# Performance work log

Measured on AMD Instinct MI355X. Metric: run time of the kernel, lower is better.

Reference implementation:

```python
import jax, jax.numpy as jnp
import numpy as np

N_NODES = 50000
N_EDGES = 800000
D_IN = 128
D_OUT = 128
N_MLP = 2


def _lin(x, W, b):
    return x @ W.T + b


def setup_inputs() -> dict:
    key = jax.random.key(0)
    ks = jax.random.split(key, 32)
    d = {}
    d['feat'] = jax.random.normal(ks[0], (N_NODES, D_IN), dtype=jnp.float32)
    d['src'] = jax.random.randint(ks[1], (N_EDGES,), 0, N_NODES, dtype=jnp.int32)
    d['dst'] = jax.random.randint(ks[2], (N_EDGES,), 0, N_NODES, dtype=jnp.int32)
    s_in = 1.0 / np.sqrt(D_IN)
    s_out = 1.0 / np.sqrt(D_OUT)
    i = 3
    def w(shape, s):
        nonlocal i
        out = jax.random.normal(ks[i], shape, dtype=jnp.float32) * s
        i += 1
        return out
    for nm in ['asrc', 'adst', 'asub', 'amul']:
        d['W_' + nm] = w((D_OUT, D_IN), s_in)
        d['b_' + nm] = w((D_OUT,), s_in)
    d['W_aout'] = w((1, D_OUT), s_out)
    d['b_aout'] = w((1,), s_out)
    for nm in ['pool', 'pool2']:
        d['W_' + nm] = w((D_IN, D_IN), s_in)
        d['b_' + nm] = w((D_IN,), s_in)
    for nm in ['self', 'neigh', 'neigh2']:
        d['W_' + nm] = w((D_OUT, D_IN), s_in)
        d['b_' + nm] = w((D_OUT,), s_in)
    d['W_mlp'] = w((N_MLP, D_OUT, D_OUT), s_out)
    d['b_mlp'] = w((N_MLP, D_OUT), s_out)
    return d


def reference(feat, src, dst,
              W_asrc, b_asrc, W_adst, b_adst, W_asub, b_asub, W_amul, b_amul,
              W_aout, b_aout, W_pool, b_pool, W_pool2, b_pool2,
              W_self, b_self, W_neigh, b_neigh, W_neigh2, b_neigh2,
              W_mlp, b_mlp):
    gelu = lambda x: jax.nn.gelu(x, approximate=False)
    fs = feat[src]            # [E, D_IN] gathered source feats
    fd = feat[dst]            # [E, D_IN] gathered dest feats
    # edge attention score
    e = _lin(fs - fd, W_asub, b_asub) + _lin(fs * fd, W_amul, b_amul)
    e = e + _lin(feat, W_asrc, b_asrc)[src] + _lin(feat, W_adst, b_adst)[dst]
    e = gelu(e)
    e = jax.nn.leaky_relu(_lin(e, W_aout, b_aout), 0.2)  # [E, 1]
    deg = jax.ops.segment_sum(jnp.ones((src.shape[0],), jnp.float32), dst,
                              num_segments=N_NODES)      # in-degree
    has_in = (deg > 0)[:, None]
    # max-pool branch
    h = gelu(_lin(feat, W_pool, b_pool))
    m = e * h[src]
    neigh = jax.ops.segment_max(m, dst, num_segments=N_NODES)
    neigh = jnp.where(has_in, neigh, 0.0)
    # mean-pool branch
    h2 = gelu(_lin(feat, W_pool2, b_pool2))
    m2 = e * h2[src]
    neigh2 = jax.ops.segment_sum(m2, dst, num_segments=N_NODES)
    neigh2 = neigh2 / jnp.maximum(deg, 1.0)[:, None]
    rst = _lin(feat, W_self, b_self) + _lin(neigh, W_neigh, b_neigh) \
        + _lin(neigh2, W_neigh2, b_neigh2)
    for li in range(W_mlp.shape[0]):
        rst = rst + _lin(gelu(rst), W_mlp[li], b_mlp[li])
    return rst
```

## Files before the change

### kernel.cpp

```cpp
#include <hip/hip_runtime.h>
#include <cstdint>
#include <cstddef>

#define NN 50000
#define NE 800000
#define DD 128

#define NBK 391
#define BSLOT 4096

static_assert(NN % 16 == 0, "node tiles");
static_assert(NE % 16 == 0, "edge tiles");
static_assert(((NN + 127) >> 7) == NBK, "bucket count");

typedef _Float16 h16_t;
typedef h16_t h16x8 __attribute__((ext_vector_type(8)));
typedef h16_t h16x4 __attribute__((ext_vector_type(4)));
typedef float f32x4 __attribute__((ext_vector_type(4)));
typedef float f32x16 __attribute__((ext_vector_type(16)));

__device__ __forceinline__ float gelu_f(float x) {
    float u = x * x;
    float t = fmaf(u, -0.1029442445f, -2.3021184019f);
    float s = __builtin_amdgcn_exp2f(x * t);
    return x * __builtin_amdgcn_rcpf(1.0f + s);
}

__device__ __forceinline__ int frag_idx(int ch, int k) {
    int t = ch >> 4, n = ch & 15;
    int kb = k >> 5, r = k & 31, q = r >> 3, j = r & 7;
    return ((((t * 4 + kb) * 4 + q) * 16 + n) << 3) + j;
}

__device__ __forceinline__ int frag32_idx(int ch, int k) {
    int t = ch >> 5, m = ch & 31;
    int kc = k >> 4, q = (k >> 3) & 1, j = k & 7;
    return ((((t * 8 + kc) * 2 + q) * 32 + m) << 3) + j;
}

__global__ __launch_bounds__(256) void convert_feat_kernel(
    const float* __restrict__ feat, h16_t* __restrict__ fb)
{
    int i = blockIdx.x * 256 + threadIdx.x;
    f32x4 v = ((const f32x4*)feat)[i];
    h16x4 o;
    o[0] = (h16_t)v[0]; o[1] = (h16_t)v[1]; o[2] = (h16_t)v[2]; o[3] = (h16_t)v[3];
    ((h16x4*)fb)[i] = o;
}

__global__ __launch_bounds__(256) void prep_kernel(
    const float* __restrict__ W_asrc, const float* __restrict__ b_asrc,
    const float* __restrict__ W_adst, const float* __restrict__ b_adst,
    const float* __restrict__ W_asub, const float* __restrict__ b_asub,
    const float* __restrict__ W_amul, const float* __restrict__ b_amul,
    const float* __restrict__ W_pool, const float* __restrict__ W_pool2,
    const float* __restrict__ W_self, const float* __restrict__ b_self,
    const float* __restrict__ W_neigh, const float* __restrict__ b_neigh,
    const float* __restrict__ W_neigh2, const float* __restrict__ b_neigh2,
    const float* __restrict__ W_mlp,
    h16_t* __restrict__ W_Sf, h16_t* __restrict__ W_Df, h16_t* __restrict__ W_amulf,
    h16_t* __restrict__ W_poolf, h16_t* __restrict__ W_pool2f,
    h16_t* __restrict__ W_selff, h16_t* __restrict__ W_neighf, h16_t* __restrict__ W_neigh2f,
    h16_t* __restrict__ W_mlpf,
    float* __restrict__ b_e, float* __restrict__ b_rst)
{
    int gid = blockIdx.x * 256 + threadIdx.x;
    float sub = W_asub[gid];
    int ch = gid >> 7, k = gid & 127;
    int fi = frag_idx(ch, k);
    W_Sf[fi] = (h16_t)(W_asrc[gid] + sub);
    W_Df[fi] = (h16_t)(W_adst[gid] - sub);
    W_amulf[frag32_idx(ch, k)] = (h16_t)W_amul[gid];
    W_poolf[fi]   = (h16_t)W_pool[gid];
    W_pool2f[fi]  = (h16_t)W_pool2[gid];
    W_selff[fi]   = (h16_t)W_self[gid];
    W_neighf[fi]  = (h16_t)W_neigh[gid];
    W_neigh2f[fi] = (h16_t)W_neigh2[gid];
    W_mlpf[fi]            = (h16_t)W_mlp[gid];
    W_mlpf[DD * DD + fi]  = (h16_t)W_mlp[DD * DD + gid];
    if (gid < DD) {
        b_e[gid]   = b_asub[gid] + b_amul[gid] + b_asrc[gid] + b_adst[gid];
        b_rst[gid] = b_self[gid] + b_neigh[gid] + b_neigh2[gid];
    }
}

__global__ __launch_bounds__(256) void scatter_bucket_kernel(
    const int* __restrict__ src, const int* __restrict__ dst,
    int* __restrict__ gcursor, int2* __restrict__ ebuf)
{
    __shared__ int cnt[NBK];
    __shared__ int ofs[NBK];
    int t = threadIdx.x;
    for (int b = t; b < NBK; b += 256) cnt[b] = 0;
    __syncthreads();
    int qbase = blockIdx.x * 1024 + t;
    int4 s4[4], d4[4];
    bool valid[4];
#pragma unroll
    for (int k = 0; k < 4; k++) {
        int q = qbase + k * 256;
        valid[k] = q < NE / 4;
        if (valid[k]) {
            s4[k] = ((const int4*)src)[q];
            d4[k] = ((const int4*)dst)[q];
#pragma unroll
            for (int j = 0; j < 4; j++)
                atomicAdd(&cnt[((&d4[k].x)[j]) >> 7], 1);
        }
    }
    __syncthreads();
    for (int b = t; b < NBK; b += 256) {
        int c = cnt[b];
        ofs[b] = c ? atomicAdd(&gcursor[b], c) : 0;
    }
    __syncthreads();
#pragma unroll
    for (int k = 0; k < 4; k++) {
        if (valid[k]) {
#pragma unroll
            for (int j = 0; j < 4; j++) {
                int d = (&d4[k].x)[j];
                int b = d >> 7;
                int p = atomicAdd(&ofs[b], 1);
                int2 pk;
                pk.x = (&s4[k].x)[j];
                pk.y = d;
                ebuf[(size_t)b * BSLOT + p] = pk;
            }
        }
    }
}

__global__ __launch_bounds__(256) void finalize_csr_kernel(
    const int2* __restrict__ ebuf, const int* __restrict__ gcursor,
    int2* __restrict__ csr, int* __restrict__ offsets, int* __restrict__ deg)
{
    __shared__ int lcnt[128];
    __shared__ int nbase[128];
    __shared__ int pre[128];
    __shared__ int redbuf[256];
    int B = blockIdx.x, t = threadIdx.x;
    int v0 = B << 7;
    int cnt = gcursor[B];
    int partial = 0;
    for (int i = t; i < B; i += 256) partial += gcursor[i];
    redbuf[t] = partial;
    __syncthreads();
#pragma unroll
    for (int d = 128; d > 0; d >>= 1) {
        if (t < d) redbuf[t] += redbuf[t + d];
        __syncthreads();
    }
    int dbase = redbuf[0];
    const int2* eb = ebuf + (size_t)B * BSLOT;
    if (t < 128) lcnt[t] = 0;
    __syncthreads();
    for (int i = t; i < cnt; i += 256)
        atomicAdd(&lcnt[eb[i].y - v0], 1);
    __syncthreads();
    int c = (t < 128) ? lcnt[t] : 0;
    if (t < 128) pre[t] = c;
    __syncthreads();
#pragma unroll
    for (int d = 1; d < 128; d <<= 1) {
        int x = (t >= d && t < 128) ? pre[t - d] : 0;
        __syncthreads();
        if (t < 128) pre[t] += x;
        __syncthreads();
    }
    if (t < 128) {
        int nb = dbase + pre[t] - c;
        nbase[t] = nb;
        int v = v0 + t;
        if (v < NN) { offsets[v] = nb; deg[v] = c; }
        lcnt[t] = 0;
    }
    __syncthreads();
    for (int i = t; i < cnt; i += 256) {
        int2 pk = eb[i];
        int j = pk.y - v0;
        int pos = nbase[j] + atomicAdd(&lcnt[j], 1);
        csr[pos] = pk;
    }
}

template <bool GELU>
__device__ __forceinline__ void mm16_to_lds(
    const h16x8 a[4], const h16_t* __restrict__ Wf, const float* __restrict__ bias,
    h16_t* __restrict__ L, int n, int q, int lane)
{
#pragma unroll
    for (int t = 0; t < 8; t++) {
        f32x4 acc = {0.f, 0.f, 0.f, 0.f};
#pragma unroll
        for (int kb = 0; kb < 4; kb++) {
            h16x8 b = *(const h16x8*)(Wf + (((t * 4 + kb) * 64 + lane) << 3));
            acc = __builtin_amdgcn_mfma_f32_16x16x32_f16(a[kb], b, acc, 0, 0, 0);
        }
        int ch = t * 16 + n;
        float bv = bias ? bias[ch] : 0.0f;
#pragma unroll
        for (int r = 0; r < 4; r++) {
            float v = acc[r] + bv;
            L[(q * 4 + r) * 136 + ch] = (h16_t)(GELU ? gelu_f(v) : v);
        }
    }
}

__global__ __launch_bounds__(256) void node_linear_kernel(
    const h16_t* __restrict__ fb,
    const h16_t* __restrict__ W_poolf, const float* __restrict__ b_pool,
    const h16_t* __restrict__ W_pool2f, const float* __restrict__ b_pool2,
    const h16_t* __restrict__ W_Sf, const float* __restrict__ b_e,
    const h16_t* __restrict__ W_Df,
    h16_t* __restrict__ hh, h16_t* __restrict__ us, h16_t* __restrict__ ud)
{
    __shared__ __align__(16) h16_t Lh[4][16 * 136];
    __shared__ __align__(16) h16_t Lh2[4][16 * 136];
    int wave = threadIdx.x >> 6;
    int wid = blockIdx.x * 4 + wave;
    if (wid >= NN / 16) return;
    int lane = threadIdx.x & 63, n = lane & 15, q = lane >> 4;
    int nb = wid * 16;
    h16_t* lh = Lh[wave];
    h16_t* lh2 = Lh2[wave];
    h16x8 a[4];
#pragma unroll
    for (int kb = 0; kb < 4; kb++)
        a[kb] = *(const h16x8*)(fb + (size_t)(nb + n) * DD + kb * 32 + q * 8);

    mm16_to_lds<true>(a, W_poolf, b_pool, lh, n, q, lane);
    mm16_to_lds<true>(a, W_pool2f, b_pool2, lh2, n, q, lane);
    __builtin_amdgcn_wave_barrier();
#pragma unroll
    for (int i = 0; i < 8; i++) {
        int r = 2 * i + (lane >> 5);
        int c = lane & 31;
        h16x4 xh = *(const h16x4*)(lh + r * 136 + 4 * c);
        h16x4 x2 = *(const h16x4*)(lh2 + r * 136 + 4 * c);
        h16x8 o;
        o[0] = xh[0]; o[1] = xh[1]; o[2] = x2[0]; o[3] = x2[1];
        o[4] = xh[2]; o[5] = xh[3]; o[6] = x2[2]; o[7] = x2[3];
        *(h16x8*)(hh + (size_t)(nb + r) * 256 + 8 * c) = o;
    }
    __builtin_amdgcn_wave_barrier();
    mm16_to_lds<false>(a, W_Sf, b_e, lh, n, q, lane);
    __builtin_amdgcn_wave_barrier();
#pragma unroll
    for (int i = 0; i < 4; i++) {
        int r = 4 * i + (lane >> 4);
        int c = lane & 15;
        *(h16x8*)(us + (size_t)(nb + r) * 128 + 8 * c) = *(const h16x8*)(lh + r * 136 + 8 * c);
    }
    __builtin_amdgcn_wave_barrier();
    mm16_to_lds<false>(a, W_Df, nullptr, lh, n, q, lane);
    __builtin_amdgcn_wave_barrier();
#pragma unroll
    for (int i = 0; i < 4; i++) {
        int r = 4 * i + (lane >> 4);
        int c = lane & 15;
        *(h16x8*)(ud + (size_t)(nb + r) * 128 + 8 * c) = *(const h16x8*)(lh + r * 136 + 8 * c);
    }
}

#define ES_NBLK 2500
#define ES_ITERS (NE / 32 / ES_NBLK)

__global__ __launch_bounds__(256, 4) void edge_score_kernel(
    const h16_t* __restrict__ fb,
    const h16_t* __restrict__ us, const h16_t* __restrict__ ud,
    const h16_t* __restrict__ W_amulf,
    const float* __restrict__ w_aout, const float* __restrict__ b_aout,
    int2* __restrict__ csr)
{
    __shared__ __align__(16) h16_t sP[32 * 128];
    __shared__ __align__(16) h16_t sU[32 * 128];
    __shared__ float partials[32 * 5];
    __shared__ float sWa[128];
    int tid = threadIdx.x;
    int wave = tid >> 6, lane = tid & 63;
    int n = lane & 31, q = lane >> 5;
    int t = wave;

    if (tid < 128) sWa[tid] = w_aout[tid];

    h16x8 wAm[8];
#pragma unroll
    for (int kc = 0; kc < 8; kc++)
        wAm[kc] = *(const h16x8*)(W_amulf + ((((t * 8 + kc) * 2 + q) * 32 + n) << 3));
    float bout = b_aout[0];

    int sed0 = tid >> 4, sc = tid & 15;

    int e0 = blockIdx.x * 32;
    int2 pk0 = csr[e0 + sed0];
    int2 pk1 = csr[e0 + sed0 + 16];
    h16x8 pfs0 = *(const h16x8*)(fb + (size_t)pk0.x * DD + sc * 8);
    h16x8 pfd0 = *(const h16x8*)(fb + (size_t)pk0.y * DD + sc * 8);
    h16x8 pus0 = *(const h16x8*)(us + (size_t)pk0.x * DD + sc * 8);
    h16x8 pud0 = *(const h16x8*)(ud + (size_t)pk0.y * DD + sc * 8);
    h16x8 pfs1 = *(const h16x8*)(fb + (size_t)pk1.x * DD + sc * 8);
    h16x8 pfd1 = *(const h16x8*)(fb + (size_t)pk1.y * DD + sc * 8);
    h16x8 pus1 = *(const h16x8*)(us + (size_t)pk1.x * DD + sc * 8);
    h16x8 pud1 = *(const h16x8*)(ud + (size_t)pk1.y * DD + sc * 8);

    for (int it = 0; it < ES_ITERS; it++) {
        int eb = (blockIdx.x + it * ES_NBLK) * 32;
        {
            h16x8 pp = pfs0 * pfd0;
            h16x8 uu = pus0 + pud0;
            int ph = (sc ^ (sed0 & 7)) << 3;
            *(h16x8*)(sP + sed0 * 128 + ph) = pp;
            *(h16x8*)(sU + sed0 * 128 + ph) = uu;
        }
        {
            int ed = sed0 + 16;
            h16x8 pp = pfs1 * pfd1;
            h16x8 uu = pus1 + pud1;
            int ph = (sc ^ (ed & 7)) << 3;
            *(h16x8*)(sP + ed * 128 + ph) = pp;
            *(h16x8*)(sU + ed * 128 + ph) = uu;
        }
        __syncthreads();
        if (it + 1 < ES_ITERS) {
            int e1 = (blockIdx.x + (it + 1) * ES_NBLK) * 32;
            pk0 = csr[e1 + sed0];
            pk1 = csr[e1 + sed0 + 16];
            pfs0 = *(const h16x8*)(fb + (size_t)pk0.x * DD + sc * 8);
            pfd0 = *(const h16x8*)(fb + (size_t)pk0.y * DD + sc * 8);
            pus0 = *(const h16x8*)(us + (size_t)pk0.x * DD + sc * 8);
            pud0 = *(const h16x8*)(ud + (size_t)pk0.y * DD + sc * 8);
            pfs1 = *(const h16x8*)(fb + (size_t)pk1.x * DD + sc * 8);
            pfd1 = *(const h16x8*)(fb + (size_t)pk1.y * DD + sc * 8);
            pus1 = *(const h16x8*)(us + (size_t)pk1.x * DD + sc * 8);
            pud1 = *(const h16x8*)(ud + (size_t)pk1.y * DD + sc * 8);
        }
        f32x16 acc = {};
        int swz = n & 7;
#pragma unroll
        for (int kc = 0; kc < 8; kc++) {
            h16x8 bP = *(const h16x8*)(sP + n * 128 + (((kc * 2 + q) ^ swz) << 3));
            acc = __builtin_amdgcn_mfma_f32_32x32x16_f16(wAm[kc], bP, acc, 0, 0, 0);
        }
        float psum = 0.f;
#pragma unroll
        for (int c = 0; c < 4; c++) {
            h16x4 sv = *(const h16x4*)(sU + n * 128 + (((t * 4 + c) ^ swz) << 3) + q * 4);
            f32x4 wv = *(const f32x4*)(sWa + t * 32 + c * 8 + q * 4);
#pragma unroll
            for (int j = 0; j < 4; j++)
                psum = fmaf(gelu_f(acc[c * 4 + j] + (float)sv[j]), wv[j], psum);
        }
        psum += __shfl_xor(psum, 32, 64);
        if (lane < 32) partials[lane * 5 + wave] = psum;
        __syncthreads();
        if (wave == (it & 3) && lane < 32) {
            const float* pr = partials + lane * 5;
            float s = pr[0] + pr[1] + pr[2] + pr[3] + bout;
            s = s > 0.f ? s : 0.2f * s;
            csr[eb + lane].y = __float_as_int(s);
        }
    }
}

__global__ __launch_bounds__(256) void aggregate_kernel(
    const h16_t* __restrict__ hh,
    const int* __restrict__ offsets, const int* __restrict__ deg,
    const int2* __restrict__ csr,
    h16_t* __restrict__ neigh, h16_t* __restrict__ neigh2)
{
    int wave = threadIdx.x >> 6, lane = threadIdx.x & 63;
    int v = blockIdx.x * 4 + wave;
    if (v >= NN) return;
    int off = offsets[v];
    int dg = deg[v];
    int quarter = lane >> 4;
    int cl = lane & 15;
    float mx[8], sm[8];
#pragma unroll
    for (int j = 0; j < 8; j++) { mx[j] = -INFINITY; sm[j] = 0.f; }
    for (int base = 0; base < dg; base += 64) {
        int cnt = dg - base; if (cnt > 64) cnt = 64;
        int s_l = 0; float sc_l = 0.f;
        if (lane < cnt) {
            int2 pk = csr[off + base + lane];
            s_l = pk.x;
            sc_l = __int_as_float(pk.y);
        }
        int nit = (cnt + 3) >> 2;
#pragma unroll 2
        for (int i = 0; i < nit; i++) {
            int idx = 4 * i + quarter;
            int s = __shfl(s_l, idx, 64);
            float sc = __shfl(sc_l, idx, 64);
            if (idx < cnt) {
                const h16_t* row = hh + (size_t)s * 256 + 16 * cl;
                h16x8 h0 = *(const h16x8*)(row);
                h16x8 h1 = *(const h16x8*)(row + 8);
                mx[0] = fmaxf(mx[0], sc * (float)h0[0]);
                mx[1] = fmaxf(mx[1], sc * (float)h0[1]);
                sm[0] = fmaf(sc, (float)h0[2], sm[0]);
                sm[1] = fmaf(sc, (float)h0[3], sm[1]);
                mx[2] = fmaxf(mx[2], sc * (float)h0[4]);
                mx[3] = fmaxf(mx[3], sc * (float)h0[5]);
                sm[2] = fmaf(sc, (float)h0[6], sm[2]);
                sm[3] = fmaf(sc, (float)h0[7], sm[3]);
                mx[4] = fmaxf(mx[4], sc * (float)h1[0]);
                mx[5] = fmaxf(mx[5], sc * (float)h1[1]);
                sm[4] = fmaf(sc, (float)h1[2], sm[4]);
                sm[5] = fmaf(sc, (float)h1[3], sm[5]);
                mx[6] = fmaxf(mx[6], sc * (float)h1[4]);
                mx[7] = fmaxf(mx[7], sc * (float)h1[5]);
                sm[6] = fmaf(sc, (float)h1[6], sm[6]);
                sm[7] = fmaf(sc, (float)h1[7], sm[7]);
            }
        }
    }
#pragma unroll
    for (int j = 0; j < 8; j++) {
        mx[j] = fmaxf(mx[j], __shfl_xor(mx[j], 16, 64));
        mx[j] = fmaxf(mx[j], __shfl_xor(mx[j], 32, 64));
        sm[j] += __shfl_xor(sm[j], 16, 64);
        sm[j] += __shfl_xor(sm[j], 32, 64);
    }
    if (quarter == 0) {
        float inv = 1.0f / (float)(dg > 1 ? dg : 1);
        h16x8 n1, n2;
#pragma unroll
        for (int j = 0; j < 8; j++) {
            n1[j] = (h16_t)(dg > 0 ? mx[j] : 0.0f);
            n2[j] = (h16_t)(sm[j] * inv);
        }
        *(h16x8*)(neigh + (size_t)v * DD + 8 * cl) = n1;
        *(h16x8*)(neigh2 + (size_t)v * DD + 8 * cl) = n2;
    }
}

__global__ __launch_bounds__(256) void final_kernel(
    const h16_t* __restrict__ fb, const h16_t* __restrict__ neigh, const h16_t* __restrict__ neigh2,
    const h16_t* __restrict__ W_selff, const h16_t* __restrict__ W_neighf, const h16_t* __restrict__ W_neigh2f,
    const float* __restrict__ b_rst,
    const h16_t* __restrict__ W_mlpf, const float* __restrict__ b_mlp,
    float* __restrict__ out)
{
    __shared__ __align__(16) float lds[4][16 * 132];
    int wave = threadIdx.x >> 6;
    int wid = blockIdx.x * 4 + wave;
    if (wid >= NN / 16) return;
    int lane = threadIdx.x & 63, n = lane & 15, q = lane >> 4;
    int nb = wid * 16;
    float* L = lds[wave];

    h16x8 af[4], an[4], am[4];
#pragma unroll
    for (int kb = 0; kb < 4; kb++) {
        size_t o = (size_t)(nb + n) * DD + kb * 32 + q * 8;
        af[kb] = *(const h16x8*)(fb + o);
        an[kb] = *(const h16x8*)(neigh + o);
        am[kb] = *(const h16x8*)(neigh2 + o);
    }
    f32x4 rst[8];
#pragma unroll
    for (int t = 0; t < 8; t++) {
        f32x4 acc = {0.f, 0.f, 0.f, 0.f};
#pragma unroll
        for (int kb = 0; kb < 4; kb++) {
            int wo = ((t * 4 + kb) * 64 + lane) << 3;
            acc = __builtin_amdgcn_mfma_f32_16x16x32_f16(af[kb], *(const h16x8*)(W_selff + wo), acc, 0, 0, 0);
            acc = __builtin_amdgcn_mfma_f32_16x16x32_f16(an[kb], *(const h16x8*)(W_neighf + wo), acc, 0, 0, 0);
            acc = __builtin_amdgcn_mfma_f32_16x16x32_f16(am[kb], *(const h16x8*)(W_neigh2f + wo), acc, 0, 0, 0);
        }
        float bv = b_rst[t * 16 + n];
#pragma unroll
        for (int r = 0; r < 4; r++) acc[r] += bv;
        rst[t] = acc;
    }

#pragma unroll
    for (int li = 0; li < 2; li++) {
#pragma unroll
        for (int t = 0; t < 8; t++)
#pragma unroll
            for (int r = 0; r < 4; r++)
                L[(q * 4 + r) * 132 + t * 16 + n] = gelu_f(rst[t][r]);
        __builtin_amdgcn_wave_barrier();
        h16x8 g[4];
#pragma unroll
        for (int kb = 0; kb < 4; kb++) {
            const f32x4* p = (const f32x4*)&L[n * 132 + kb * 32 + q * 8];
            f32x4 x0 = p[0], x1 = p[1];
            h16x8 gg;
            gg[0] = (h16_t)x0[0]; gg[1] = (h16_t)x0[1]; gg[2] = (h16_t)x0[2]; gg[3] = (h16_t)x0[3];
            gg[4] = (h16_t)x1[0]; gg[5] = (h16_t)x1[1]; gg[6] = (h16_t)x1[2]; gg[7] = (h16_t)x1[3];
            g[kb] = gg;
        }
        __builtin_amdgcn_wave_barrier();
        const h16_t* Wl = W_mlpf + li * DD * DD;
#pragma unroll
        for (int t = 0; t < 8; t++) {
            f32x4 acc = {0.f, 0.f, 0.f, 0.f};
#pragma unroll
            for (int kb = 0; kb < 4; kb++) {
                h16x8 b = *(const h16x8*)(Wl + (((t * 4 + kb) * 64 + lane) << 3));
                acc = __builtin_amdgcn_mfma_f32_16x16x32_f16(g[kb], b, acc, 0, 0, 0);
            }
            float bm = b_mlp[li * DD + t * 16 + n];
#pragma unroll
            for (int r = 0; r < 4; r++) rst[t][r] += acc[r] + bm;
        }
    }

#pragma unroll
    for (int t = 0; t < 8; t++)
#pragma unroll
        for (int r = 0; r < 4; r++)
            out[(size_t)(nb + q * 4 + r) * DD + t * 16 + n] = rst[t][r];
}

extern "C" void kernel_launch(void* const* d_in, const int* in_sizes, int n_in,
                              void* d_out, int out_size, void* d_ws, size_t ws_size,
                              hipStream_t stream)
{
    const float* feat    = (const float*)d_in[0];
    const int*   src     = (const int*)d_in[1];
    const int*   dst     = (const int*)d_in[2];
    const float* W_asrc  = (const float*)d_in[3],  *b_asrc  = (const float*)d_in[4];
    const float* W_adst  = (const float*)d_in[5],  *b_adst  = (const float*)d_in[6];
    const float* W_asub  = (const float*)d_in[7],  *b_asub  = (const float*)d_in[8];
    const float* W_amul  = (const float*)d_in[9],  *b_amul  = (const float*)d_in[10];
    const float* W_aout  = (const float*)d_in[11], *b_aout  = (const float*)d_in[12];
    const float* W_pool  = (const float*)d_in[13], *b_pool  = (const float*)d_in[14];
    const float* W_pool2 = (const float*)d_in[15], *b_pool2 = (const float*)d_in[16];
    const float* W_self  = (const float*)d_in[17], *b_self  = (const float*)d_in[18];
    const float* W_neigh = (const float*)d_in[19], *b_neigh = (const float*)d_in[20];
    const float* W_neigh2= (const float*)d_in[21], *b_neigh2= (const float*)d_in[22];
    const float* W_mlp   = (const float*)d_in[23], *b_mlp   = (const float*)d_in[24];
    float* out = (float*)d_out;

    char* w = (char*)d_ws;
    auto take = [&](size_t bytes) -> void* {
        void* p = (void*)w;
        w += (bytes + 255) & ~(size_t)255;
        return p;
    };
    h16_t* fb      = (h16_t*)take((size_t)NN * DD * sizeof(h16_t));
    h16_t* neigh   = (h16_t*)take((size_t)NN * DD * sizeof(h16_t));
    h16_t* neigh2  = (h16_t*)take((size_t)NN * DD * sizeof(h16_t));
    h16_t* hh      = (h16_t*)take((size_t)NN * 256 * sizeof(h16_t));
    h16_t* us      = (h16_t*)take((size_t)NN * DD * sizeof(h16_t));
    h16_t* ud      = (h16_t*)take((size_t)NN * DD * sizeof(h16_t));
    int*    deg     = (int*)take((size_t)NN * sizeof(int));
    int*    offsets = (int*)take((size_t)NN * sizeof(int));
    int2*   csr     = (int2*)take((size_t)NE * sizeof(int2));
    int2*   ebuf    = (int2*)take((size_t)NBK * BSLOT * sizeof(int2));
    int*    gcursor = (int*)take((size_t)NBK * sizeof(int));
    h16_t* W_Sf    = (h16_t*)take((size_t)DD * DD * sizeof(h16_t));
    h16_t* W_Df    = (h16_t*)take((size_t)DD * DD * sizeof(h16_t));
    h16_t* W_amulf = (h16_t*)take((size_t)DD * DD * sizeof(h16_t));
    h16_t* W_poolf = (h16_t*)take((size_t)DD * DD * sizeof(h16_t));
    h16_t* W_pool2f= (h16_t*)take((size_t)DD * DD * sizeof(h16_t));
    h16_t* W_selff = (h16_t*)take((size_t)DD * DD * sizeof(h16_t));
    h16_t* W_neighf= (h16_t*)take((size_t)DD * DD * sizeof(h16_t));
    h16_t* W_neigh2f=(h16_t*)take((size_t)DD * DD * sizeof(h16_t));
    h16_t* W_mlpf  = (h16_t*)take((size_t)2 * DD * DD * sizeof(h16_t));
    float*  b_e     = (float*)take((size_t)DD * sizeof(float));
    float*  b_rst   = (float*)take((size_t)DD * sizeof(float));

    (void)hipMemsetAsync(gcursor, 0, (size_t)NBK * sizeof(int), stream);

    convert_feat_kernel<<<NN * DD / 4 / 256, 256, 0, stream>>>(feat, fb);

    prep_kernel<<<DD * DD / 256, 256, 0, stream>>>(
        W_asrc, b_asrc, W_adst, b_adst, W_asub, b_asub, W_amul, b_amul,
        W_pool, W_pool2, W_self, b_self, W_neigh, b_neigh, W_neigh2, b_neigh2, W_mlp,
        W_Sf, W_Df, W_amulf, W_poolf, W_pool2f, W_selff, W_neighf, W_neigh2f, W_mlpf,
        b_e, b_rst);

    scatter_bucket_kernel<<<(NE / 4 + 1023) / 1024, 256, 0, stream>>>(src, dst, gcursor, ebuf);
    finalize_csr_kernel<<<NBK, 256, 0, stream>>>(ebuf, gcursor, csr, offsets, deg);

    const int nwaves = NN / 16;
    const int ngrid = (nwaves + 3) / 4;
    node_linear_kernel<<<ngrid, 256, 0, stream>>>(
        fb, W_poolf, b_pool, W_pool2f, b_pool2, W_Sf, b_e, W_Df, hh, us, ud);

    edge_score_kernel<<<ES_NBLK, 256, 0, stream>>>(
        fb, us, ud, W_amulf, W_aout, b_aout, csr);

    aggregate_kernel<<<(NN + 3) / 4, 256, 0, stream>>>(
        hh, offsets, deg, csr, neigh, neigh2);

    final_kernel<<<ngrid, 256, 0, stream>>>(
        fb, neigh, neigh2, W_selff, W_neighf, W_neigh2f, b_rst, W_mlpf, b_mlp, out);
}
```

Baseline: 345.0 us.

## Compute source projection per edge with MFMA instead of gathering precomputed us

Drops the per-node us = feat·W_S projection from the node-linear kernel and instead applies W_S to the gathered source features inside the edge-score MFMA loop, alongside the W_amul product. This removes one 128-wide fp16 gather per edge plus the us write and read traffic. In exchange it doubles the MFMA work per edge, keeps eight more weight fragments in registers and adds an LDS tile and a bias add, which may hurt occupancy under the four-blocks-per-SM launch bound.

New measurement: 387.4 us. +12.3%, slower.

```diff
diff --git a/kernel.cpp b/kernel.cpp
--- a/kernel.cpp
+++ b/kernel.cpp
@@ -68,9 +68,10 @@
     float sub = W_asub[gid];
     int ch = gid >> 7, k = gid & 127;
     int fi = frag_idx(ch, k);
-    W_Sf[fi] = (h16_t)(W_asrc[gid] + sub);
+    int fi32 = frag32_idx(ch, k);
+    W_Sf[fi32] = (h16_t)(W_asrc[gid] + sub);
     W_Df[fi] = (h16_t)(W_adst[gid] - sub);
-    W_amulf[frag32_idx(ch, k)] = (h16_t)W_amul[gid];
+    W_amulf[fi32] = (h16_t)W_amul[gid];
     W_poolf[fi]   = (h16_t)W_pool[gid];
     W_pool2f[fi]  = (h16_t)W_pool2[gid];
     W_selff[fi]   = (h16_t)W_self[gid];
@@ -211,9 +212,8 @@
     const h16_t* __restrict__ fb,
     const h16_t* __restrict__ W_poolf, const float* __restrict__ b_pool,
     const h16_t* __restrict__ W_pool2f, const float* __restrict__ b_pool2,
-    const h16_t* __restrict__ W_Sf, const float* __restrict__ b_e,
     const h16_t* __restrict__ W_Df,
-    h16_t* __restrict__ hh, h16_t* __restrict__ us, h16_t* __restrict__ ud)
+    h16_t* __restrict__ hh, h16_t* __restrict__ ud)
 {
     __shared__ __align__(16) h16_t Lh[4][16 * 136];
     __shared__ __align__(16) h16_t Lh2[4][16 * 136];
@@ -244,15 +244,6 @@
         *(h16x8*)(hh + (size_t)(nb + r) * 256 + 8 * c) = o;
     }
     __builtin_amdgcn_wave_barrier();
-    mm16_to_lds<false>(a, W_Sf, b_e, lh, n, q, lane);
-    __builtin_amdgcn_wave_barrier();
-#pragma unroll
-    for (int i = 0; i < 4; i++) {
-        int r = 4 * i + (lane >> 4);
-        int c = lane & 15;
-        *(h16x8*)(us + (size_t)(nb + r) * 128 + 8 * c) = *(const h16x8*)(lh + r * 136 + 8 * c);
-    }
-    __builtin_amdgcn_wave_barrier();
     mm16_to_lds<false>(a, W_Df, nullptr, lh, n, q, lane);
     __builtin_amdgcn_wave_barrier();
 #pragma unroll
@@ -267,27 +258,32 @@
 #define ES_ITERS (NE / 32 / ES_NBLK)
 
 __global__ __launch_bounds__(256, 4) void edge_score_kernel(
-    const h16_t* __restrict__ fb,
-    const h16_t* __restrict__ us, const h16_t* __restrict__ ud,
-    const h16_t* __restrict__ W_amulf,
+    const h16_t* __restrict__ fb, const h16_t* __restrict__ ud,
+    const h16_t* __restrict__ W_amulf, const h16_t* __restrict__ W_Sf,
     const float* __restrict__ w_aout, const float* __restrict__ b_aout,
+    const float* __restrict__ b_e,
     int2* __restrict__ csr)
 {
     __shared__ __align__(16) h16_t sP[32 * 128];
+    __shared__ __align__(16) h16_t sS[32 * 128];
     __shared__ __align__(16) h16_t sU[32 * 128];
     __shared__ float partials[32 * 5];
     __shared__ float sWa[128];
+    __shared__ float sBe[128];
     int tid = threadIdx.x;
     int wave = tid >> 6, lane = tid & 63;
     int n = lane & 31, q = lane >> 5;
     int t = wave;
 
-    if (tid < 128) sWa[tid] = w_aout[tid];
-
-    h16x8 wAm[8];
-#pragma unroll
-    for (int kc = 0; kc < 8; kc++)
-        wAm[kc] = *(const h16x8*)(W_amulf + ((((t * 8 + kc) * 2 + q) * 32 + n) << 3));
+    if (tid < 128) { sWa[tid] = w_aout[tid]; sBe[tid] = b_e[tid]; }
+
+    h16x8 wAm[8], wSf[8];
+#pragma unroll
+    for (int kc = 0; kc < 8; kc++) {
+        int wo = (((t * 8 + kc) * 2 + q) * 32 + n) << 3;
+        wAm[kc] = *(const h16x8*)(W_amulf + wo);
+        wSf[kc] = *(const h16x8*)(W_Sf + wo);
+    }
     float bout = b_aout[0];
 
     int sed0 = tid >> 4, sc = tid & 15;
@@ -297,29 +293,27 @@
     int2 pk1 = csr[e0 + sed0 + 16];
     h16x8 pfs0 = *(const h16x8*)(fb + (size_t)pk0.x * DD + sc * 8);
     h16x8 pfd0 = *(const h16x8*)(fb + (size_t)pk0.y * DD + sc * 8);
-    h16x8 pus0 = *(const h16x8*)(us + (size_t)pk0.x * DD + sc * 8);
     h16x8 pud0 = *(const h16x8*)(ud + (size_t)pk0.y * DD + sc * 8);
     h16x8 pfs1 = *(const h16x8*)(fb + (size_t)pk1.x * DD + sc * 8);
     h16x8 pfd1 = *(const h16x8*)(fb + (size_t)pk1.y * DD + sc * 8);
-    h16x8 pus1 = *(const h16x8*)(us + (size_t)pk1.x * DD + sc * 8);
     h16x8 pud1 = *(const h16x8*)(ud + (size_t)pk1.y * DD + sc * 8);
 
     for (int it = 0; it < ES_ITERS; it++) {
         int eb = (blockIdx.x + it * ES_NBLK) * 32;
         {
             h16x8 pp = pfs0 * pfd0;
-            h16x8 uu = pus0 + pud0;
             int ph = (sc ^ (sed0 & 7)) << 3;
             *(h16x8*)(sP + sed0 * 128 + ph) = pp;
-            *(h16x8*)(sU + sed0 * 128 + ph) = uu;
+            *(h16x8*)(sS + sed0 * 128 + ph) = pfs0;
+            *(h16x8*)(sU + sed0 * 128 + ph) = pud0;
         }
         {
             int ed = sed0 + 16;
             h16x8 pp = pfs1 * pfd1;
-            h16x8 uu = pus1 + pud1;
             int ph = (sc ^ (ed & 7)) << 3;
             *(h16x8*)(sP + ed * 128 + ph) = pp;
-            *(h16x8*)(sU + ed * 128 + ph) = uu;
+            *(h16x8*)(sS + ed * 128 + ph) = pfs1;
+            *(h16x8*)(sU + ed * 128 + ph) = pud1;
         }
         __syncthreads();
         if (it + 1 < ES_ITERS) {
@@ -328,28 +322,28 @@
             pk1 = csr[e1 + sed0 + 16];
             pfs0 = *(const h16x8*)(fb + (size_t)pk0.x * DD + sc * 8);
             pfd0 = *(const h16x8*)(fb + (size_t)pk0.y * DD + sc * 8);
-            pus0 = *(const h16x8*)(us + (size_t)pk0.x * DD + sc * 8);
             pud0 = *(const h16x8*)(ud + (size_t)pk0.y * DD + sc * 8);
             pfs1 = *(const h16x8*)(fb + (size_t)pk1.x * DD + sc * 8);
             pfd1 = *(const h16x8*)(fb + (size_t)pk1.y * DD + sc * 8);
-            pus1 = *(const h16x8*)(us + (size_t)pk1.x * DD + sc * 8);
             pud1 = *(const h16x8*)(ud + (size_t)pk1.y * DD + sc * 8);
         }
         f32x16 acc = {};
         int swz = n & 7;
 #pragma unroll
         for (int kc = 0; kc < 8; kc++) {
-            h16x8 bP = *(const h16x8*)(sP + n * 128 + (((kc * 2 + q) ^ swz) << 3));
-            acc = __builtin_amdgcn_mfma_f32_32x32x16_f16(wAm[kc], bP, acc, 0, 0, 0);
+            int off = n * 128 + (((kc * 2 + q) ^ swz) << 3);
+            acc = __builtin_amdgcn_mfma_f32_32x32x16_f16(wAm[kc], *(const h16x8*)(sP + off), acc, 0, 0, 0);
+            acc = __builtin_amdgcn_mfma_f32_32x32x16_f16(wSf[kc], *(const h16x8*)(sS + off), acc, 0, 0, 0);
         }
         float psum = 0.f;
 #pragma unroll
         for (int c = 0; c < 4; c++) {
             h16x4 sv = *(const h16x4*)(sU + n * 128 + (((t * 4 + c) ^ swz) << 3) + q * 4);
             f32x4 wv = *(const f32x4*)(sWa + t * 32 + c * 8 + q * 4);
+            f32x4 bv = *(const f32x4*)(sBe + t * 32 + c * 8 + q * 4);
 #pragma unroll
             for (int j = 0; j < 4; j++)
-                psum = fmaf(gelu_f(acc[c * 4 + j] + (float)sv[j]), wv[j], psum);
+                psum = fmaf(gelu_f(acc[c * 4 + j] + (float)sv[j] + bv[j]), wv[j], psum);
         }
         psum += __shfl_xor(psum, 32, 64);
         if (lane < 32) partials[lane * 5 + wave] = psum;
@@ -547,7 +541,6 @@
     h16_t* neigh   = (h16_t*)take((size_t)NN * DD * sizeof(h16_t));
     h16_t* neigh2  = (h16_t*)take((size_t)NN * DD * sizeof(h16_t));
     h16_t* hh      = (h16_t*)take((size_t)NN * 256 * sizeof(h16_t));
-    h16_t* us      = (h16_t*)take((size_t)NN * DD * sizeof(h16_t));
     h16_t* ud      = (h16_t*)take((size_t)NN * DD * sizeof(h16_t));
     int*    deg     = (int*)take((size_t)NN * sizeof(int));
     int*    offsets = (int*)take((size_t)NN * sizeof(int));
@@ -582,10 +575,10 @@
     const int nwaves = NN / 16;
     const int ngrid = (nwaves + 3) / 4;
     node_linear_kernel<<<ngrid, 256, 0, stream>>>(
-        fb, W_poolf, b_pool, W_pool2f, b_pool2, W_Sf, b_e, W_Df, hh, us, ud);
+        fb, W_poolf, b_pool, W_pool2f, b_pool2, W_Df, hh, ud);
 
     edge_score_kernel<<<ES_NBLK, 256, 0, stream>>>(
-        fb, us, ud, W_amulf, W_aout, b_aout, csr);
+        fb, ud, W_amulf, W_Sf, W_aout, b_aout, b_e, csr);
 
     aggregate_kernel<<<(NN + 3) / 4, 256, 0, stream>>>(
         hh, offsets, deg, csr, neigh, neigh2);
```
